# Kernel optimization log

Hardware: AMD Instinct MI355X
Metric: run time of the kernel (lower is better)

## Reference

```python
import jax, jax.numpy as jnp
import numpy as np

D_MODEL = 1024
H = 16
D_H = D_MODEL // H


def setup_inputs() -> dict:
    key = jax.random.key(0)
    ks = jax.random.split(key, 10)
    B, T_dec, T_enc = 2, 2048, 2048
    s = 1.0 / np.sqrt(D_MODEL)
    return {
        "tgt": jax.random.normal(ks[0], (B, T_dec, D_MODEL), jnp.float32),
        "memory": jax.random.normal(ks[1], (B, T_enc, D_MODEL), jnp.float32),
        "W_q": jax.random.normal(ks[2], (D_MODEL, D_MODEL), jnp.float32) * s,
        "b_q": jnp.zeros((D_MODEL,), jnp.float32),
        "W_k": jax.random.normal(ks[3], (D_MODEL, D_MODEL), jnp.float32) * s,
        "b_k": jnp.zeros((D_MODEL,), jnp.float32),
        "W_v": jax.random.normal(ks[4], (D_MODEL, D_MODEL), jnp.float32) * s,
        "b_v": jnp.zeros((D_MODEL,), jnp.float32),
        "W_o": jax.random.normal(ks[5], (D_MODEL, D_MODEL), jnp.float32) * s,
        "b_o": jnp.zeros((D_MODEL,), jnp.float32),
    }


def reference(tgt, memory, W_q, b_q, W_k, b_k, W_v, b_v, W_o, b_o):
    B, T_dec, _ = tgt.shape
    T_enc = memory.shape[1]
    # Projections (nn.Linear: x @ W^T + b; here W stored as (in,out) so x @ W + b)
    Q = tgt @ W_q + b_q          # (B, T_dec, d_model)
    K = memory @ W_k + b_k       # (B, T_enc, d_model)
    V = memory @ W_v + b_v       # (B, T_enc, d_model)
    # split heads: (B, h, T, d_h)
    Q = Q.reshape(B, T_dec, H, D_H).transpose(0, 2, 1, 3)
    K = K.reshape(B, T_enc, H, D_H).transpose(0, 2, 1, 3)
    V = V.reshape(B, T_enc, H, D_H).transpose(0, 2, 1, 3)
    # scores (B, h, T_dec, T_enc)
    S = jnp.einsum("bhqd,bhkd->bhqk", Q, K) / jnp.sqrt(jnp.float32(D_H)).astype(Q.dtype)
    A = jax.nn.softmax(S, axis=-1)
    Y = jnp.einsum("bhqk,bhkd->bhqd", A, V)
    Y = Y.transpose(0, 2, 1, 3).reshape(B, T_dec, D_MODEL)
    return Y @ W_o + b_o
```

## Files before the change

### kernel.cpp

```cpp
#include <hip/hip_runtime.h>
#include <hip/hip_bf16.h>
#include <stdint.h>

typedef unsigned short u16;
typedef __attribute__((ext_vector_type(8))) short bf16x8;
typedef __attribute__((ext_vector_type(4))) short bf16x4;
typedef __attribute__((ext_vector_type(4))) float f32x4;

__device__ __forceinline__ float bf2f(u16 u) {
    union { unsigned int i; float f; } v; v.i = ((unsigned int)u) << 16; return v.f;
}
__device__ __forceinline__ u16 f2bf(float f) {
    union { float f; unsigned int i; } v; v.f = f;
    unsigned int x = v.i;
    return (u16)((x + 0x7fffu + ((x >> 16) & 1u)) >> 16);
}
__device__ __forceinline__ unsigned fbits(float f) {
    union { float f; unsigned int i; } v; v.f = f; return v.i;
}
__device__ __forceinline__ void async16(const void* g, void* lds) {
    __builtin_amdgcn_global_load_lds((const __attribute__((address_space(1))) void*)g,
                                     (__attribute__((address_space(3))) void*)lds,
                                     16, 0, 0);
}

#define QSCALE 0.18033688f

__global__ __launch_bounds__(256) void prep(
    const float* __restrict__ tgt, const float* __restrict__ mem,
    const float* __restrict__ Wq, const float* __restrict__ Wk,
    const float* __restrict__ Wv, const float* __restrict__ Wo,
    u16* __restrict__ Wt, u16* __restrict__ tgtb, u16* __restrict__ memb)
{
    __shared__ u16 tile[64][65];
    const int id = blockIdx.x;
    const int tid = threadIdx.x;
    if (id < 1024) {
        const int z = id >> 8;
        const float* in = (z == 0) ? Wq : (z == 1) ? Wk : (z == 2) ? Wv : Wo;
        u16* out = Wt + (size_t)z * 1048576;
        const int k0 = (id & 15) * 64, n0 = ((id >> 4) & 15) * 64;
        const int r = tid >> 2, c0 = (tid & 3) << 4;
#pragma unroll
        for (int i = 0; i < 4; ++i) {
            float4 v = *(const float4*)&in[(size_t)(k0 + r) * 1024 + n0 + c0 + i * 4];
            tile[c0 + i * 4 + 0][r] = f2bf(v.x);
            tile[c0 + i * 4 + 1][r] = f2bf(v.y);
            tile[c0 + i * 4 + 2][r] = f2bf(v.z);
            tile[c0 + i * 4 + 3][r] = f2bf(v.w);
        }
        __syncthreads();
#pragma unroll
        for (int i = 0; i < 2; ++i) {
            bf16x8 v;
#pragma unroll
            for (int j = 0; j < 8; ++j) v[j] = (short)tile[r][c0 + i * 8 + j];
            *(bf16x8*)&out[(size_t)(n0 + r) * 1024 + k0 + c0 + i * 8] = v;
        }
    } else {
        size_t i = ((size_t)(id - 1024) * 256 + tid) * 8;
        float4 a0 = *(const float4*)&tgt[i];
        float4 a1 = *(const float4*)&tgt[i + 4];
        float4 b0 = *(const float4*)&mem[i];
        float4 b1 = *(const float4*)&mem[i + 4];
        bf16x8 va, vb;
        va[0] = (short)f2bf(a0.x); va[1] = (short)f2bf(a0.y);
        va[2] = (short)f2bf(a0.z); va[3] = (short)f2bf(a0.w);
        va[4] = (short)f2bf(a1.x); va[5] = (short)f2bf(a1.y);
        va[6] = (short)f2bf(a1.z); va[7] = (short)f2bf(a1.w);
        vb[0] = (short)f2bf(b0.x); vb[1] = (short)f2bf(b0.y);
        vb[2] = (short)f2bf(b0.z); vb[3] = (short)f2bf(b0.w);
        vb[4] = (short)f2bf(b1.x); vb[5] = (short)f2bf(b1.y);
        vb[6] = (short)f2bf(b1.z); vb[7] = (short)f2bf(b1.w);
        *(bf16x8*)&tgtb[i] = va;
        *(bf16x8*)&memb[i] = vb;
    }
}

__global__ __launch_bounds__(256) void gemm_qkv(
    const u16* __restrict__ tgtb, const u16* __restrict__ memb,
    const u16* __restrict__ Wt,
    const float* __restrict__ bq, const float* __restrict__ bk, const float* __restrict__ bv,
    u16* __restrict__ Qb, u16* __restrict__ Kb, u16* __restrict__ Vtb)
{
    __shared__ __align__(16) u16 sA[2][128 * 32];
    __shared__ __align__(16) u16 sB[2][128 * 32];
    const int z = blockIdx.z;
    const u16* A = (z == 0) ? tgtb : memb;
    const u16* Bt = Wt + (size_t)z * 1048576;
    const float* bias = (z == 0) ? bq : (z == 1) ? bk : bv;

    const int tid = threadIdx.x;
    const int wave = tid >> 6, lane = tid & 63;
    const int quad = lane >> 4, l16 = lane & 15;
    const int m0 = blockIdx.x * 128, n0 = blockIdx.y * 128;
    const int wm = (wave & 1) * 64, wn = (wave >> 1) * 64;
    const int sw = (quad ^ ((l16 >> 1) & 3)) << 3;

    f32x4 acc[4][4] = {};

#define GSTAGE(k0, buf)                                                       \
    {                                                                         \
        _Pragma("unroll")                                                     \
        for (int r = 0; r < 2; ++r) {                                         \
            int c = tid + r * 256;                                            \
            int g = (c & 3) ^ ((c >> 3) & 3);                                 \
            const u16* gA = A + (size_t)(m0 + (c >> 2)) * 1024 + (k0) + g * 8;\
            async16(gA, (char*)&sA[buf][0] + r * 4096 + wave * 1024);         \
            const u16* gB = Bt + (size_t)(n0 + (c >> 2)) * 1024 + (k0) + g * 8;\
            async16(gB, (char*)&sB[buf][0] + r * 4096 + wave * 1024);         \
        }                                                                     \
    }

    GSTAGE(0, 0);
    GSTAGE(32, 1);

    for (int it = 0; it < 32; ++it) {
        if (it < 31) { asm volatile("s_waitcnt vmcnt(4)" ::: "memory"); }
        else         { asm volatile("s_waitcnt vmcnt(0)" ::: "memory"); }
        __builtin_amdgcn_sched_barrier(0);
        __builtin_amdgcn_s_barrier();
        __builtin_amdgcn_sched_barrier(0);

        const u16* a   = &sA[it & 1][0];
        const u16* bb_ = &sB[it & 1][0];
        bf16x8 af[4], bfr[4];
#pragma unroll
        for (int i = 0; i < 4; ++i) {
            af[i]  = *(const bf16x8*)&a[(wm + i * 16 + l16) * 32 + sw];
            bfr[i] = *(const bf16x8*)&bb_[(wn + i * 16 + l16) * 32 + sw];
        }
        asm volatile("s_waitcnt lgkmcnt(0)" ::: "memory");
        __builtin_amdgcn_sched_barrier(0);
        __builtin_amdgcn_s_barrier();
        __builtin_amdgcn_sched_barrier(0);

        if (it < 30) GSTAGE((it + 2) * 32, it & 1);

        __builtin_amdgcn_s_setprio(1);
#pragma unroll
        for (int i = 0; i < 4; ++i)
#pragma unroll
            for (int j = 0; j < 4; ++j)
                acc[i][j] = __builtin_amdgcn_mfma_f32_16x16x32_bf16(af[i], bfr[j], acc[i][j], 0, 0, 0);
        __builtin_amdgcn_s_setprio(0);
    }
#undef GSTAGE

    if (z == 2) {
#pragma unroll
        for (int j = 0; j < 4; ++j) {
            int n = n0 + wn + j * 16 + l16;
            float bb = bias[n];
            int d = n & 63;
#pragma unroll
            for (int i = 0; i < 4; ++i) {
                int mb = m0 + wm + i * 16 + quad * 4;
                int bh = (mb >> 11) * 16 + (n >> 6);
                bf16x4 pk;
#pragma unroll
                for (int r = 0; r < 4; ++r) pk[r] = (short)f2bf(acc[i][j][r] + bb);
                *(bf16x4*)&Vtb[(size_t)bh * 131072 + (size_t)d * 2048 + (mb & 2047)] = pk;
            }
        }
    } else {
        u16* C = (z == 0) ? Qb : Kb;
        const float scl = (z == 0) ? QSCALE : 1.0f;
#pragma unroll
        for (int j = 0; j < 4; ++j) {
            int n = n0 + wn + j * 16 + l16;
            float bb = bias[n];
#pragma unroll
            for (int i = 0; i < 4; ++i) {
                int mb = m0 + wm + i * 16 + quad * 4;
#pragma unroll
                for (int r = 0; r < 4; ++r)
                    C[(size_t)(mb + r) * 1024 + n] = f2bf((acc[i][j][r] + bb) * scl);
            }
        }
    }
}

__global__ __launch_bounds__(256) void gemm_out(
    const u16* __restrict__ A, const u16* __restrict__ Bt,
    const float* __restrict__ bias, float* __restrict__ C)
{
    __shared__ __align__(16) u16 sA[2][64 * 32];
    __shared__ __align__(16) u16 sB[2][128 * 32];
    const int tid = threadIdx.x;
    const int wave = tid >> 6, lane = tid & 63;
    const int quad = lane >> 4, l16 = lane & 15;
    const int m0 = blockIdx.x * 64, n0 = blockIdx.y * 128;
    const int wm = (wave & 1) * 32, wn = (wave >> 1) * 64;
    const int sw = (quad ^ ((l16 >> 1) & 3)) << 3;
    f32x4 acc[2][4] = {};

#define OSTAGE(k0, buf)                                                       \
    {                                                                         \
        {                                                                     \
            int c = tid;                                                      \
            int g = (c & 3) ^ ((c >> 3) & 3);                                 \
            const u16* gA = A + (size_t)(m0 + (c >> 2)) * 1024 + (k0) + g * 8;\
            async16(gA, (char*)&sA[buf][0] + wave * 1024);                    \
        }                                                                     \
        _Pragma("unroll")                                                     \
        for (int r = 0; r < 2; ++r) {                                         \
            int c = tid + r * 256;                                            \
            int g = (c & 3) ^ ((c >> 3) & 3);                                 \
            const u16* gB = Bt + (size_t)(n0 + (c >> 2)) * 1024 + (k0) + g * 8;\
            async16(gB, (char*)&sB[buf][0] + r * 4096 + wave * 1024);         \
        }                                                                     \
    }

    OSTAGE(0, 0);
    OSTAGE(32, 1);

    for (int it = 0; it < 32; ++it) {
        if (it < 31) { asm volatile("s_waitcnt vmcnt(3)" ::: "memory"); }
        else         { asm volatile("s_waitcnt vmcnt(0)" ::: "memory"); }
        __builtin_amdgcn_sched_barrier(0);
        __builtin_amdgcn_s_barrier();
        __builtin_amdgcn_sched_barrier(0);

        const u16* a   = &sA[it & 1][0];
        const u16* bb_ = &sB[it & 1][0];
        bf16x8 af[2], bfr[4];
#pragma unroll
        for (int i = 0; i < 2; ++i)
            af[i] = *(const bf16x8*)&a[(wm + i * 16 + l16) * 32 + sw];
#pragma unroll
        for (int j = 0; j < 4; ++j)
            bfr[j] = *(const bf16x8*)&bb_[(wn + j * 16 + l16) * 32 + sw];
        asm volatile("s_waitcnt lgkmcnt(0)" ::: "memory");
        __builtin_amdgcn_sched_barrier(0);
        __builtin_amdgcn_s_barrier();
        __builtin_amdgcn_sched_barrier(0);

        if (it < 30) OSTAGE((it + 2) * 32, it & 1);

        __builtin_amdgcn_s_setprio(1);
#pragma unroll
        for (int i = 0; i < 2; ++i)
#pragma unroll
            for (int j = 0; j < 4; ++j)
                acc[i][j] = __builtin_amdgcn_mfma_f32_16x16x32_bf16(af[i], bfr[j], acc[i][j], 0, 0, 0);
        __builtin_amdgcn_s_setprio(0);
    }
#undef OSTAGE

#pragma unroll
    for (int j = 0; j < 4; ++j) {
        int n = n0 + wn + j * 16 + l16;
        float bb = bias[n];
#pragma unroll
        for (int i = 0; i < 2; ++i) {
            int mb = m0 + wm + i * 16 + quad * 4;
#pragma unroll
            for (int r = 0; r < 4; ++r)
                C[(size_t)(mb + r) * 1024 + n] = acc[i][j][r] + bb;
        }
    }
}

__global__ __launch_bounds__(256, 2) void attn_kernel(
    const u16* __restrict__ Q,
    const u16* __restrict__ K,
    const u16* __restrict__ Vt,
    u16* __restrict__ Y)
{
    __shared__ __align__(16) u16 sK[2][4096];
    __shared__ __align__(16) u16 sV[2][4096];

    const int tid = threadIdx.x;
    const int wave = tid >> 6, lane = tid & 63;
    const int quad = lane >> 4, l16 = lane & 15;

    const int bidx = blockIdx.x;
    const int bh = (bidx & 7) * 4 + ((bidx >> 3) & 3);
    const int qt = bidx >> 5;
    const int b = bh >> 4, h = bh & 15;
    const size_t qrow0 = (size_t)b * 2048 + qt * 128;
    const int st = ((qt << 1) | (bh & 1)) & 31;

    const size_t qrowA = qrow0 + wave * 32 + l16;
    const size_t qrowB = qrowA + 16;
    bf16x8 qA0 = *(const bf16x8*)&Q[qrowA * 1024 + h * 64 + quad * 8];
    bf16x8 qA1 = *(const bf16x8*)&Q[qrowA * 1024 + h * 64 + 32 + quad * 8];
    bf16x8 qB0 = *(const bf16x8*)&Q[qrowB * 1024 + h * 64 + quad * 8];
    bf16x8 qB1 = *(const bf16x8*)&Q[qrowB * 1024 + h * 64 + 32 + quad * 8];

    f32x4 oA[4] = {}, oB[4] = {};
    float rowA = 0.0f, rowB = 0.0f;

    const u16* Kbase = K + (size_t)b * 2048 * 1024 + h * 64;
    const u16* Vbase = Vt + (size_t)bh * 131072;

    const int x7 = l16 & 7;
    int koff[2], voff[4];
#pragma unroll
    for (int kf = 0; kf < 2; ++kf)
        koff[kf] = (l16 * 8 + ((kf * 4 + quad) ^ x7)) * 8;
#pragma unroll
    for (int ks = 0; ks < 4; ++ks)
        voff[ks] = (l16 * 8 + ((ks * 2 + (quad >> 1)) ^ x7)) * 8 + (quad & 1) * 4;

#define STAGE1(kv0, buf, r)                                                   \
    {                                                                         \
        int c = tid + (r) * 256;                                              \
        int srow = c >> 3;                                                    \
        int g = (c & 7) ^ (srow & 7);                                         \
        async16(Kbase + (size_t)((kv0) + srow) * 1024 + g * 8,                \
                (char*)&sK[buf][0] + (r) * 4096 + wave * 1024);               \
        async16(Vbase + (size_t)srow * 2048 + (kv0) + g * 8,                  \
                (char*)&sV[buf][0] + (r) * 4096 + wave * 1024);               \
    }
#define STAGE(kv0, buf) STAGE1(kv0, buf, 0) STAGE1(kv0, buf, 1)

    STAGE(st * 64, 0);

    for (int i = 0; i < 32; ++i) {
        __syncthreads();
        if (i < 31) {
            int kvn = ((st + i + 1) & 31) * 64;
            STAGE(kvn, (i + 1) & 1);
        }
        const u16* kb = &sK[i & 1][0];
        const u16* vb = &sV[i & 1][0];

        bf16x8 kfr[4][2];
        bf16x4 vfr[4][4];
#pragma unroll
        for (int ks = 0; ks < 4; ++ks) {
            kfr[ks][0] = *(const bf16x8*)&kb[ks * 1024 + koff[0]];
            kfr[ks][1] = *(const bf16x8*)&kb[ks * 1024 + koff[1]];
        }
#pragma unroll
        for (int mt = 0; mt < 4; ++mt)
#pragma unroll
            for (int ks = 0; ks < 4; ++ks)
                vfr[mt][ks] = *(const bf16x4*)&vb[mt * 1024 + voff[ks]];

        __builtin_amdgcn_s_setprio(1);
#pragma unroll
        for (int ks = 0; ks < 4; ++ks) {
            f32x4 sA = {0.f, 0.f, 0.f, 0.f};
            f32x4 sB = {0.f, 0.f, 0.f, 0.f};
            sA = __builtin_amdgcn_mfma_f32_16x16x32_bf16(kfr[ks][0], qA0, sA, 0, 0, 0);
            sB = __builtin_amdgcn_mfma_f32_16x16x32_bf16(kfr[ks][0], qB0, sB, 0, 0, 0);
            sA = __builtin_amdgcn_mfma_f32_16x16x32_bf16(kfr[ks][1], qA1, sA, 0, 0, 0);
            sB = __builtin_amdgcn_mfma_f32_16x16x32_bf16(kfr[ks][1], qB1, sB, 0, 0, 0);
            float a0 = __builtin_amdgcn_exp2f(sA[0]);
            float a1 = __builtin_amdgcn_exp2f(sA[1]);
            float a2 = __builtin_amdgcn_exp2f(sA[2]);
            float a3 = __builtin_amdgcn_exp2f(sA[3]);
            float b0 = __builtin_amdgcn_exp2f(sB[0]);
            float b1 = __builtin_amdgcn_exp2f(sB[1]);
            float b2 = __builtin_amdgcn_exp2f(sB[2]);
            float b3 = __builtin_amdgcn_exp2f(sB[3]);
            rowA += (a0 + a1) + (a2 + a3);
            rowB += (b0 + b1) + (b2 + b3);
            unsigned loA = __builtin_amdgcn_perm(fbits(a1) + 0x8000u, fbits(a0) + 0x8000u, 0x07060302u);
            unsigned hiA = __builtin_amdgcn_perm(fbits(a3) + 0x8000u, fbits(a2) + 0x8000u, 0x07060302u);
            unsigned loB = __builtin_amdgcn_perm(fbits(b1) + 0x8000u, fbits(b0) + 0x8000u, 0x07060302u);
            unsigned hiB = __builtin_amdgcn_perm(fbits(b3) + 0x8000u, fbits(b2) + 0x8000u, 0x07060302u);
            union { unsigned u[2]; bf16x4 v; } pA, pB;
            pA.u[0] = loA; pA.u[1] = hiA;
            pB.u[0] = loB; pB.u[1] = hiB;
#pragma unroll
            for (int mt = 0; mt < 4; ++mt) {
                oA[mt] = __builtin_amdgcn_mfma_f32_16x16x16bf16_1k(vfr[mt][ks], pA.v, oA[mt], 0, 0, 0);
                oB[mt] = __builtin_amdgcn_mfma_f32_16x16x16bf16_1k(vfr[mt][ks], pB.v, oB[mt], 0, 0, 0);
            }
        }
        __builtin_amdgcn_s_setprio(0);
    }
#undef STAGE
#undef STAGE1

    rowA += __shfl_xor(rowA, 16, 64);
    rowA += __shfl_xor(rowA, 32, 64);
    rowB += __shfl_xor(rowB, 16, 64);
    rowB += __shfl_xor(rowB, 32, 64);
    const float invA = 1.0f / rowA;
    const float invB = 1.0f / rowB;

#pragma unroll
    for (int mt = 0; mt < 4; ++mt) {
        bf16x4 oa, ob;
#pragma unroll
        for (int r = 0; r < 4; ++r) {
            oa[r] = (short)f2bf(oA[mt][r] * invA);
            ob[r] = (short)f2bf(oB[mt][r] * invB);
        }
        *(bf16x4*)&Y[qrowA * 1024 + h * 64 + mt * 16 + quad * 4] = oa;
        *(bf16x4*)&Y[qrowB * 1024 + h * 64 + mt * 16 + quad * 4] = ob;
    }
}

extern "C" void kernel_launch(void* const* d_in, const int* in_sizes, int n_in,
                              void* d_out, int out_size, void* d_ws, size_t ws_size,
                              hipStream_t stream) {
    const float* tgt = (const float*)d_in[0];
    const float* mem = (const float*)d_in[1];
    const float* Wq  = (const float*)d_in[2];
    const float* bq  = (const float*)d_in[3];
    const float* Wk  = (const float*)d_in[4];
    const float* bk  = (const float*)d_in[5];
    const float* Wv  = (const float*)d_in[6];
    const float* bv  = (const float*)d_in[7];
    const float* Wo  = (const float*)d_in[8];
    const float* bo  = (const float*)d_in[9];

    u16* ws = (u16*)d_ws;
    const size_t SZ = 4194304;
    u16* Wt   = ws;
    u16* tgtb = ws + 4 * SZ;
    u16* memb = tgtb + SZ;
    u16* Qb   = memb + SZ;
    u16* Kb   = Qb + SZ;
    u16* Vtb  = Kb + SZ;
    u16* Yb   = Vtb + SZ;
    float* out = (float*)d_out;

    prep<<<dim3(3072), 256, 0, stream>>>(tgt, mem, Wq, Wk, Wv, Wo, Wt, tgtb, memb);
    gemm_qkv<<<dim3(32, 8, 3), 256, 0, stream>>>(tgtb, memb, Wt, bq, bk, bv, Qb, Kb, Vtb);
    attn_kernel<<<dim3(512), 256, 0, stream>>>(Qb, Kb, Vtb, Yb);
    gemm_out<<<dim3(64, 8), 256, 0, stream>>>(Yb, Wt + 3 * (size_t)1048576, bo, out);
}
```

Before: 209.9 us.

## Fuse K and V projections into one block sharing the memory A tile

Measured after the change: 201.7 us. -3.9%, faster.

```diff
diff --git a/kernel.cpp b/kernel.cpp
--- a/kernel.cpp
+++ b/kernel.cpp
@@ -77,18 +77,19 @@
     }
 }
 
-__global__ __launch_bounds__(256) void gemm_qkv(
+__global__ __launch_bounds__(256, 2) void gemm_qkv(
     const u16* __restrict__ tgtb, const u16* __restrict__ memb,
     const u16* __restrict__ Wt,
     const float* __restrict__ bq, const float* __restrict__ bk, const float* __restrict__ bv,
     u16* __restrict__ Qb, u16* __restrict__ Kb, u16* __restrict__ Vtb)
 {
     __shared__ __align__(16) u16 sA[2][128 * 32];
-    __shared__ __align__(16) u16 sB[2][128 * 32];
+    __shared__ __align__(16) u16 sBk[2][128 * 32];
+    __shared__ __align__(16) u16 sBv[2][128 * 32];
     const int z = blockIdx.z;
-    const u16* A = (z == 0) ? tgtb : memb;
-    const u16* Bt = Wt + (size_t)z * 1048576;
-    const float* bias = (z == 0) ? bq : (z == 1) ? bk : bv;
+    const u16* A  = (z == 0) ? tgtb : memb;
+    const u16* B0 = (z == 0) ? Wt : (Wt + 1048576);
+    const u16* B1 = Wt + 2097152;
 
     const int tid = threadIdx.x;
     const int wave = tid >> 6, lane = tid & 63;
@@ -97,7 +98,8 @@
     const int wm = (wave & 1) * 64, wn = (wave >> 1) * 64;
     const int sw = (quad ^ ((l16 >> 1) & 3)) << 3;
 
-    f32x4 acc[4][4] = {};
+    f32x4 accK[4][4] = {};
+    f32x4 accV[4][4] = {};
 
 #define GSTAGE(k0, buf)                                                       \
     {                                                                         \
@@ -107,8 +109,12 @@
             int g = (c & 3) ^ ((c >> 3) & 3);                                 \
             const u16* gA = A + (size_t)(m0 + (c >> 2)) * 1024 + (k0) + g * 8;\
             async16(gA, (char*)&sA[buf][0] + r * 4096 + wave * 1024);         \
-            const u16* gB = Bt + (size_t)(n0 + (c >> 2)) * 1024 + (k0) + g * 8;\
-            async16(gB, (char*)&sB[buf][0] + r * 4096 + wave * 1024);         \
+            const u16* gB = B0 + (size_t)(n0 + (c >> 2)) * 1024 + (k0) + g * 8;\
+            async16(gB, (char*)&sBk[buf][0] + r * 4096 + wave * 1024);        \
+            if (z) {                                                          \
+                const u16* gV = B1 + (size_t)(n0 + (c >> 2)) * 1024 + (k0) + g * 8;\
+                async16(gV, (char*)&sBv[buf][0] + r * 4096 + wave * 1024);    \
+            }                                                                 \
         }                                                                     \
     }
 
@@ -116,19 +122,27 @@
     GSTAGE(32, 1);
 
     for (int it = 0; it < 32; ++it) {
-        if (it < 31) { asm volatile("s_waitcnt vmcnt(4)" ::: "memory"); }
-        else         { asm volatile("s_waitcnt vmcnt(0)" ::: "memory"); }
+        if (it < 31) {
+            if (z) { asm volatile("s_waitcnt vmcnt(6)" ::: "memory"); }
+            else   { asm volatile("s_waitcnt vmcnt(4)" ::: "memory"); }
+        } else     { asm volatile("s_waitcnt vmcnt(0)" ::: "memory"); }
         __builtin_amdgcn_sched_barrier(0);
         __builtin_amdgcn_s_barrier();
         __builtin_amdgcn_sched_barrier(0);
 
-        const u16* a   = &sA[it & 1][0];
-        const u16* bb_ = &sB[it & 1][0];
-        bf16x8 af[4], bfr[4];
+        const u16* a  = &sA[it & 1][0];
+        const u16* b0 = &sBk[it & 1][0];
+        const u16* b1 = &sBv[it & 1][0];
+        bf16x8 af[4], bfK[4], bfV[4];
 #pragma unroll
         for (int i = 0; i < 4; ++i) {
             af[i]  = *(const bf16x8*)&a[(wm + i * 16 + l16) * 32 + sw];
-            bfr[i] = *(const bf16x8*)&bb_[(wn + i * 16 + l16) * 32 + sw];
+            bfK[i] = *(const bf16x8*)&b0[(wn + i * 16 + l16) * 32 + sw];
+        }
+        if (z) {
+#pragma unroll
+            for (int i = 0; i < 4; ++i)
+                bfV[i] = *(const bf16x8*)&b1[(wn + i * 16 + l16) * 32 + sw];
         }
         asm volatile("s_waitcnt lgkmcnt(0)" ::: "memory");
         __builtin_amdgcn_sched_barrier(0);
@@ -142,16 +156,48 @@
         for (int i = 0; i < 4; ++i)
 #pragma unroll
             for (int j = 0; j < 4; ++j)
-                acc[i][j] = __builtin_amdgcn_mfma_f32_16x16x32_bf16(af[i], bfr[j], acc[i][j], 0, 0, 0);
+                accK[i][j] = __builtin_amdgcn_mfma_f32_16x16x32_bf16(af[i], bfK[j], accK[i][j], 0, 0, 0);
+        if (z) {
+#pragma unroll
+            for (int i = 0; i < 4; ++i)
+#pragma unroll
+                for (int j = 0; j < 4; ++j)
+                    accV[i][j] = __builtin_amdgcn_mfma_f32_16x16x32_bf16(af[i], bfV[j], accV[i][j], 0, 0, 0);
+        }
         __builtin_amdgcn_s_setprio(0);
     }
 #undef GSTAGE
 
-    if (z == 2) {
+    if (z == 0) {
 #pragma unroll
         for (int j = 0; j < 4; ++j) {
             int n = n0 + wn + j * 16 + l16;
-            float bb = bias[n];
+            float bb = bq[n];
+#pragma unroll
+            for (int i = 0; i < 4; ++i) {
+                int mb = m0 + wm + i * 16 + quad * 4;
+#pragma unroll
+                for (int r = 0; r < 4; ++r)
+                    Qb[(size_t)(mb + r) * 1024 + n] = f2bf((accK[i][j][r] + bb) * QSCALE);
+            }
+        }
+    } else {
+#pragma unroll
+        for (int j = 0; j < 4; ++j) {
+            int n = n0 + wn + j * 16 + l16;
+            float bb = bk[n];
+#pragma unroll
+            for (int i = 0; i < 4; ++i) {
+                int mb = m0 + wm + i * 16 + quad * 4;
+#pragma unroll
+                for (int r = 0; r < 4; ++r)
+                    Kb[(size_t)(mb + r) * 1024 + n] = f2bf(accK[i][j][r] + bb);
+            }
+        }
+#pragma unroll
+        for (int j = 0; j < 4; ++j) {
+            int n = n0 + wn + j * 16 + l16;
+            float bb = bv[n];
             int d = n & 63;
 #pragma unroll
             for (int i = 0; i < 4; ++i) {
@@ -159,23 +205,8 @@
                 int bh = (mb >> 11) * 16 + (n >> 6);
                 bf16x4 pk;
 #pragma unroll
-                for (int r = 0; r < 4; ++r) pk[r] = (short)f2bf(acc[i][j][r] + bb);
+                for (int r = 0; r < 4; ++r) pk[r] = (short)f2bf(accV[i][j][r] + bb);
                 *(bf16x4*)&Vtb[(size_t)bh * 131072 + (size_t)d * 2048 + (mb & 2047)] = pk;
-            }
-        }
-    } else {
-        u16* C = (z == 0) ? Qb : Kb;
-        const float scl = (z == 0) ? QSCALE : 1.0f;
-#pragma unroll
-        for (int j = 0; j < 4; ++j) {
-            int n = n0 + wn + j * 16 + l16;
-            float bb = bias[n];
-#pragma unroll
-            for (int i = 0; i < 4; ++i) {
-                int mb = m0 + wm + i * 16 + quad * 4;
-#pragma unroll
-                for (int r = 0; r < 4; ++r)
-                    C[(size_t)(mb + r) * 1024 + n] = f2bf((acc[i][j][r] + bb) * scl);
             }
         }
     }
@@ -423,7 +454,7 @@
     float* out = (float*)d_out;
 
     prep<<<dim3(3072), 256, 0, stream>>>(tgt, mem, Wq, Wk, Wv, Wo, Wt, tgtb, memb);
-    gemm_qkv<<<dim3(32, 8, 3), 256, 0, stream>>>(tgtb, memb, Wt, bq, bk, bv, Qb, Kb, Vtb);
+    gemm_qkv<<<dim3(32, 8, 2), 256, 0, stream>>>(tgtb, memb, Wt, bq, bk, bv, Qb, Kb, Vtb);
     attn_kernel<<<dim3(512), 256, 0, stream>>>(Qb, Kb, Vtb, Yb);
     gemm_out<<<dim3(64, 8), 256, 0, stream>>>(Yb, Wt + 3 * (size_t)1048576, bo, out);
 }
```
